# Kernel optimization log

Hardware: AMD Instinct MI355X
Metric: run time of the kernel (lower is better)

## Reference

```python
import jax, jax.numpy as jnp
import numpy as np
import math

L = 16
DECAY = math.exp(-1.0 / 10.0)   # exp(-dt/tau)
THRESHOLD = 1.0
ALPHA = 0.01
EPS = 1e-6


def spike_fn(x):
    # MultiBitSurrogate forward: floor then clamp to [0, L]
    return jnp.clip(jnp.floor(x), 0.0, float(L))


def setup_inputs() -> dict:
    key = jax.random.key(0)
    k1, k2 = jax.random.split(key)
    B, S, D, H = 8, 4096, 512, 512
    x = jax.random.normal(k1, (B, S, D), dtype=jnp.float32)
    W = jax.random.normal(k2, (H, D), dtype=jnp.float32) * (1.0 / math.sqrt(D))
    b = jnp.zeros((H,), dtype=jnp.float32)
    return {"x": x, "W": W, "b": b}


def reference(x, W, b):
    B, S, D = x.shape
    H = W.shape[0]
    # dense input current for all timesteps: (B, S, H)
    h = jnp.einsum('bsd,hd->bsh', x, W) + b

    v0 = jnp.zeros((B, H), dtype=x.dtype)
    theta0 = jnp.full((B, H), THRESHOLD, dtype=x.dtype)

    def step(carry, i_t):
        v, theta = carry
        v = v * DECAY + i_t
        clamp_limit = L * theta * 2.0
        v = jnp.clip(v, -clamp_limit, clamp_limit)
        normalized_v = v / (theta + EPS)
        spike = spike_fn(normalized_v)
        v = v - spike * theta
        theta = theta + ALPHA * spike - ALPHA * (theta - THRESHOLD)
        return (v, theta), spike

    h_t = jnp.swapaxes(h, 0, 1)  # (S, B, H) for scan over time
    (v, theta), spikes = jax.lax.scan(step, (v0, theta0), h_t)
    spikes = jnp.swapaxes(spikes, 0, 1)  # (B, S, H)
    return spikes, v, theta
```

## Files before the change

kernel.cpp:

```cpp
#include <hip/hip_runtime.h>

#define B_DIM 8
#define S_LEN 4096
#define D_DIM 512
#define H_DIM 512

#define DECAY_F 0.90483743f
#define ALPHA_F 0.01f
#define EPS_F   1e-6f

#define KT 16
#define NCHUNK (S_LEN / 32)
#define NSCAN_BLOCKS 64


__device__ __forceinline__ void stage_chunk(const float* __restrict__ gio, float* dstbase,
                                            int c, int lane) {
    const float* src = gio + (size_t)(c * 32 + (lane >> 4)) * H_DIM + ((lane & 15) << 2);
#pragma unroll
    for (int i = 0; i < 8; ++i) {
        __builtin_amdgcn_global_load_lds(
            (const __attribute__((address_space(1))) void*)(src + (size_t)i * 4 * H_DIM),
            (__attribute__((address_space(3))) void*)(dstbase + i * 256),
            16, 0, 0);
    }
}

__device__ __forceinline__ void gemm_tile(const float* __restrict__ x,
                                          const float* __restrict__ W,
                                          const float* __restrict__ bias,
                                          float* __restrict__ out,
                                          float (*As)[132], float (*Bs)[132],
                                          int bm, int bn) {
    const int tid = threadIdx.x;
    const int waveId = tid >> 6;
    const int waveR = waveId & 1;
    const int waveC = waveId >> 1;
    const int lane = tid & 63;
    const int tr = lane >> 3;
    const int tc = lane & 7;
    const int rbase = waveR * 64 + tr * 8;
    const int c0 = waveC * 64 + tc * 4;
    const int c1 = c0 + 32;

    const int lrow = tid >> 2;
    const int lk4  = (tid & 3) * 4;

    const float* xa = &x[(size_t)(bm + lrow) * D_DIM + lk4];
    const float* xb = &x[(size_t)(bm + lrow + 64) * D_DIM + lk4];
    const float* wa = &W[(size_t)(bn + lrow) * D_DIM + lk4];
    const float* wb = &W[(size_t)(bn + lrow + 64) * D_DIM + lk4];

    float acc[8][8];
#pragma unroll
    for (int i = 0; i < 8; ++i)
#pragma unroll
        for (int j = 0; j < 8; ++j) acc[i][j] = 0.f;

    float4 a0 = *reinterpret_cast<const float4*>(xa);
    float4 a1 = *reinterpret_cast<const float4*>(xb);
    float4 b0 = *reinterpret_cast<const float4*>(wa);
    float4 b1 = *reinterpret_cast<const float4*>(wb);

    for (int kk = 0; kk < D_DIM; kk += KT) {
        __syncthreads();
        As[lk4 + 0][lrow]      = a0.x;
        As[lk4 + 1][lrow]      = a0.y;
        As[lk4 + 2][lrow]      = a0.z;
        As[lk4 + 3][lrow]      = a0.w;
        As[lk4 + 0][lrow + 64] = a1.x;
        As[lk4 + 1][lrow + 64] = a1.y;
        As[lk4 + 2][lrow + 64] = a1.z;
        As[lk4 + 3][lrow + 64] = a1.w;
        Bs[lk4 + 0][lrow]      = b0.x;
        Bs[lk4 + 1][lrow]      = b0.y;
        Bs[lk4 + 2][lrow]      = b0.z;
        Bs[lk4 + 3][lrow]      = b0.w;
        Bs[lk4 + 0][lrow + 64] = b1.x;
        Bs[lk4 + 1][lrow + 64] = b1.y;
        Bs[lk4 + 2][lrow + 64] = b1.z;
        Bs[lk4 + 3][lrow + 64] = b1.w;
        __syncthreads();

        if (kk + KT < D_DIM) {
            a0 = *reinterpret_cast<const float4*>(xa + kk + KT);
            a1 = *reinterpret_cast<const float4*>(xb + kk + KT);
            b0 = *reinterpret_cast<const float4*>(wa + kk + KT);
            b1 = *reinterpret_cast<const float4*>(wb + kk + KT);
        }

#pragma unroll
        for (int k = 0; k < KT; ++k) {
            const float4 av0 = *reinterpret_cast<const float4*>(&As[k][rbase]);
            const float4 av1 = *reinterpret_cast<const float4*>(&As[k][rbase + 4]);
            const float4 bv0 = *reinterpret_cast<const float4*>(&Bs[k][c0]);
            const float4 bv1 = *reinterpret_cast<const float4*>(&Bs[k][c1]);
            const float am[8]  = {av0.x, av0.y, av0.z, av0.w, av1.x, av1.y, av1.z, av1.w};
            const float bn_[8] = {bv0.x, bv0.y, bv0.z, bv0.w, bv1.x, bv1.y, bv1.z, bv1.w};
#pragma unroll
            for (int i = 0; i < 8; ++i)
#pragma unroll
                for (int j = 0; j < 8; ++j) acc[i][j] += am[i] * bn_[j];
        }
    }

    const float4 bias0 = *reinterpret_cast<const float4*>(&bias[bn + c0]);
    const float4 bias1 = *reinterpret_cast<const float4*>(&bias[bn + c1]);
    const float bb[8] = {bias0.x, bias0.y, bias0.z, bias0.w, bias1.x, bias1.y, bias1.z, bias1.w};

#pragma unroll
    for (int i = 0; i < 8; ++i) {
        const size_t row = (size_t)(bm + rbase + i);
        float4 o0, o1;
        o0.x = acc[i][0] + bb[0]; o0.y = acc[i][1] + bb[1];
        o0.z = acc[i][2] + bb[2]; o0.w = acc[i][3] + bb[3];
        o1.x = acc[i][4] + bb[4]; o1.y = acc[i][5] + bb[5];
        o1.z = acc[i][6] + bb[6]; o1.w = acc[i][7] + bb[7];
        *reinterpret_cast<float4*>(&out[row * H_DIM + bn + c0]) = o0;
        *reinterpret_cast<float4*>(&out[row * H_DIM + bn + c1]) = o1;
    }
}

__device__ __forceinline__ void scan_wave(float* __restrict__ gio, float* sbuf,
                                          const int* flagrow, int lane,
                                          float* __restrict__ vout,
                                          float* __restrict__ thout, int chain) {
    float v = 0.f;
    float theta = 1.f;
    float tden = theta + EPS_F;
    float rs = __builtin_amdgcn_rcpf(tden);
    float es = fmaf(-tden, rs, 1.0f);
    float r1 = fmaf(es, rs, rs);
    float es2 = fmaf(-tden, r1, 1.0f);
    float r0 = fmaf(es2, r1, r1);
    float cl = 32.f * theta;
    const float kSixteen = 16.0f;

    if (flagrow) {
        while (__hip_atomic_load(&flagrow[0], __ATOMIC_ACQUIRE, __HIP_MEMORY_SCOPE_AGENT) < 4)
            __builtin_amdgcn_s_sleep(1);
    }
    stage_chunk(gio, sbuf, 0, lane);
    asm volatile("s_waitcnt vmcnt(0)" ::: "memory");

    for (int c = 0; c < NCHUNK; ++c) {
        if (c + 1 < NCHUNK) {
            if (((c + 1) & 3) == 0 && flagrow) {
                const int stn = (c + 1) >> 2;
                while (__hip_atomic_load(&flagrow[stn], __ATOMIC_ACQUIRE,
                                         __HIP_MEMORY_SCOPE_AGENT) < 4)
                    __builtin_amdgcn_s_sleep(1);
                asm volatile("s_waitcnt vmcnt(0)" ::: "memory");
                stage_chunk(gio, sbuf + ((c + 1) & 1) * 2048, c + 1, lane);
            } else {
                stage_chunk(gio, sbuf + ((c + 1) & 1) * 2048, c + 1, lane);
                asm volatile("s_waitcnt vmcnt(40)" ::: "memory");
            }
        } else {
            asm volatile("s_waitcnt vmcnt(32)" ::: "memory");
        }
        __builtin_amdgcn_sched_barrier(0);

        const float* sb = sbuf + (c & 1) * 2048 + lane;
        float rr[32];
#pragma unroll
        for (int i = 0; i < 32; ++i) rr[i] = sb[i * 64];
        __builtin_amdgcn_sched_barrier(0);

        float* gout = gio + (size_t)c * 32 * H_DIM + lane;

#pragma unroll
        for (int u = 0; u < 32; ++u) {
            float vv = v * DECAY_F + rr[u];
            asm("v_med3_f32 %0, %0, -%1, %1" : "+v"(vv) : "v"(cl));
            v = vv;

            const float q0 = v * r0;
            const float e1 = fmaf(-tden, q0, v);
            const float nv = fmaf(e1, r0, q0);

            float spike = floorf(nv);
            asm("v_med3_f32 %0, %0, 0, %1" : "+v"(spike) : "v"(kSixteen));

            v = v - spike * theta;
            theta = theta + ALPHA_F * spike - ALPHA_F * (theta - 1.0f);

            tden = theta + EPS_F;
            const float rrcp = __builtin_amdgcn_rcpf(tden);
            const float ee = fmaf(-tden, rrcp, 1.0f);
            const float ra = fmaf(ee, rrcp, rrcp);
            const float ee2 = fmaf(-tden, ra, 1.0f);
            r0 = fmaf(ee2, ra, ra);
            cl = 32.f * theta;

            gout[(size_t)u * H_DIM] = spike;
        }
        __builtin_amdgcn_sched_barrier(0);
    }

    vout[chain]  = v;
    thout[chain] = theta;
}

__global__ __launch_bounds__(256) void fused_kernel(const float* __restrict__ x,
                                                    const float* __restrict__ W,
                                                    const float* __restrict__ bias,
                                                    float* __restrict__ out,
                                                    float* __restrict__ vout,
                                                    float* __restrict__ thout,
                                                    int* __restrict__ flags) {
    __shared__ __align__(16) char smem_raw[16896];
    const int bid = blockIdx.x;

    if (bid >= NSCAN_BLOCKS) {
        float (*As)[132] = reinterpret_cast<float (*)[132]>(smem_raw);
        float (*Bs)[132] = reinterpret_cast<float (*)[132]>(smem_raw + sizeof(float) * KT * 132);

        const int g  = bid - NSCAN_BLOCKS;
        const int st = g >> 5;
        const int bb = (g >> 2) & 7;
        const int nt = g & 3;
        const int bm = bb * S_LEN + st * 128;
        const int bn = nt * 128;

        gemm_tile(x, W, bias, out, As, Bs, bm, bn);

        __syncthreads();
        if (threadIdx.x == 0) {
            __hip_atomic_fetch_add(&flags[bb * 32 + st], 1,
                                   __ATOMIC_RELEASE, __HIP_MEMORY_SCOPE_AGENT);
        }
        return;
    }

    if (threadIdx.x >= 64) return;
    __builtin_amdgcn_s_setprio(1);

    const int lane = threadIdx.x;
    const int gi   = bid;
    const int b    = gi >> 3;
    const int h0   = (gi & 7) << 6;

    float* sbuf = reinterpret_cast<float*>(smem_raw);
    const int* flagrow = flags + b * 32;
    float* gio = out + (size_t)b * S_LEN * H_DIM + h0;
    const int chain = b * H_DIM + h0 + lane;

    scan_wave(gio, sbuf, flagrow, lane, vout, thout, chain);
}


__global__ __launch_bounds__(256) void gemm_kernel(const float* __restrict__ x,
                                                   const float* __restrict__ W,
                                                   const float* __restrict__ bias,
                                                   float* __restrict__ out) {
    __shared__ float As[KT][132];
    __shared__ float Bs[KT][132];
    const int bm = blockIdx.y * 128;
    const int bn = blockIdx.x * 128;
    gemm_tile(x, W, bias, out, As, Bs, bm, bn);
}

__global__ __launch_bounds__(64, 1) void scan_kernel(float* __restrict__ io,
                                                     float* __restrict__ vout,
                                                     float* __restrict__ thout) {
    __shared__ float sbuf[2][32][64];
    const int lane = threadIdx.x;
    const int bi = blockIdx.x;
    const int b = bi >> 3;
    const int h0 = (bi & 7) << 6;
    float* gio = io + (size_t)b * S_LEN * H_DIM + h0;
    const int chain = b * H_DIM + h0 + lane;
    scan_wave(gio, &sbuf[0][0][0], nullptr, lane, vout, thout, chain);
}

extern "C" void kernel_launch(void* const* d_in, const int* in_sizes, int n_in,
                              void* d_out, int out_size, void* d_ws, size_t ws_size,
                              hipStream_t stream) {
    const float* x    = (const float*)d_in[0];
    const float* W    = (const float*)d_in[1];
    const float* bias = (const float*)d_in[2];

    float* out   = (float*)d_out;
    float* vout  = out + (size_t)B_DIM * S_LEN * H_DIM;
    float* thout = vout + B_DIM * H_DIM;

    if (ws_size >= 1024) {
        int* flags = (int*)d_ws;
        hipMemsetAsync(flags, 0, 256 * sizeof(int), stream);
        fused_kernel<<<NSCAN_BLOCKS + 1024, 256, 0, stream>>>(x, W, bias, out,
                                                              vout, thout, flags);
    } else {
        dim3 grid(H_DIM / 128, (B_DIM * S_LEN) / 128);
        gemm_kernel<<<grid, 256, 0, stream>>>(x, W, bias, out);
        scan_kernel<<<64, 64, 0, stream>>>(out, vout, thout);
    }
}
```

Before: 334.1 us.

## Interleave two scan chains per wave and halve scan block count

Each scan wave now carries two independent recurrence chains (128 hidden columns) instead of one, interleaving their steps to hide the serial dependency latency through instruction-level parallelism. The number of scan blocks drops from 64 to 32, and chunks shrink to 16 timesteps so the shared staging buffer keeps the same size. The cost is twice the serial work per wave, on half as many waves, with higher register pressure, so total scan latency depends on whether the dual-chain ILP hides the per-step latency.

```diff
diff --git a/kernel.cpp b/kernel.cpp
--- a/kernel.cpp
+++ b/kernel.cpp
@@ -10,21 +10,8 @@
 #define EPS_F   1e-6f
 
 #define KT 16
-#define NCHUNK (S_LEN / 32)
-#define NSCAN_BLOCKS 64
-
-
-__device__ __forceinline__ void stage_chunk(const float* __restrict__ gio, float* dstbase,
-                                            int c, int lane) {
-    const float* src = gio + (size_t)(c * 32 + (lane >> 4)) * H_DIM + ((lane & 15) << 2);
-#pragma unroll
-    for (int i = 0; i < 8; ++i) {
-        __builtin_amdgcn_global_load_lds(
-            (const __attribute__((address_space(1))) void*)(src + (size_t)i * 4 * H_DIM),
-            (__attribute__((address_space(3))) void*)(dstbase + i * 256),
-            16, 0, 0);
-    }
-}
+#define NCHUNK 256
+#define NSCAN_BLOCKS 32
 
 __device__ __forceinline__ void gemm_tile(const float* __restrict__ x,
                                           const float* __restrict__ W,
@@ -121,39 +108,56 @@
     }
 }
 
-__device__ __forceinline__ void scan_wave(float* __restrict__ gio, float* sbuf,
-                                          const int* flagrow, int lane,
-                                          float* __restrict__ vout,
-                                          float* __restrict__ thout, int chain) {
-    float v = 0.f;
-    float theta = 1.f;
-    float tden = theta + EPS_F;
-    float rs = __builtin_amdgcn_rcpf(tden);
-    float es = fmaf(-tden, rs, 1.0f);
-    float r1 = fmaf(es, rs, rs);
-    float es2 = fmaf(-tden, r1, 1.0f);
-    float r0 = fmaf(es2, r1, r1);
-    float cl = 32.f * theta;
+__device__ __forceinline__ void scan_block(float* __restrict__ gio,
+                                           float* sbuf, const int* flagrow, int lane,
+                                           float* __restrict__ vout,
+                                           float* __restrict__ thout, int chainA) {
+#define SSTATE(sfx)                                                   \
+    float v##sfx = 0.f;                                               \
+    float theta##sfx = 1.f;                                           \
+    float tden##sfx = theta##sfx + EPS_F;                             \
+    float rs##sfx = __builtin_amdgcn_rcpf(tden##sfx);                 \
+    float es##sfx = fmaf(-tden##sfx, rs##sfx, 1.0f);                  \
+    float r1##sfx = fmaf(es##sfx, rs##sfx, rs##sfx);                  \
+    float es2##sfx = fmaf(-tden##sfx, r1##sfx, 1.0f);                 \
+    float r0##sfx = fmaf(es2##sfx, r1##sfx, r1##sfx);                 \
+    float cl##sfx = 32.f * theta##sfx;
+    SSTATE(A)
+    SSTATE(B)
+#undef SSTATE
     const float kSixteen = 16.0f;
+
+#define STAGE16(DST, C)                                                              \
+    do {                                                                             \
+        const float* src_ = gio + (size_t)((C) * 16 + (lane >> 5)) * H_DIM           \
+                              + ((lane & 31) << 2);                                  \
+        _Pragma("unroll")                                                            \
+        for (int i_ = 0; i_ < 8; ++i_) {                                             \
+            __builtin_amdgcn_global_load_lds(                                        \
+                (const __attribute__((address_space(1))) void*)(src_ + (size_t)(2 * i_) * H_DIM), \
+                (__attribute__((address_space(3))) void*)((DST) + i_ * 256),         \
+                16, 0, 0);                                                           \
+        }                                                                            \
+    } while (0)
 
     if (flagrow) {
         while (__hip_atomic_load(&flagrow[0], __ATOMIC_ACQUIRE, __HIP_MEMORY_SCOPE_AGENT) < 4)
             __builtin_amdgcn_s_sleep(1);
     }
-    stage_chunk(gio, sbuf, 0, lane);
+    STAGE16(sbuf, 0);
     asm volatile("s_waitcnt vmcnt(0)" ::: "memory");
 
     for (int c = 0; c < NCHUNK; ++c) {
         if (c + 1 < NCHUNK) {
-            if (((c + 1) & 3) == 0 && flagrow) {
-                const int stn = (c + 1) >> 2;
+            if (((c + 1) & 7) == 0 && flagrow) {
+                const int stn = (c + 1) >> 3;
                 while (__hip_atomic_load(&flagrow[stn], __ATOMIC_ACQUIRE,
                                          __HIP_MEMORY_SCOPE_AGENT) < 4)
                     __builtin_amdgcn_s_sleep(1);
                 asm volatile("s_waitcnt vmcnt(0)" ::: "memory");
-                stage_chunk(gio, sbuf + ((c + 1) & 1) * 2048, c + 1, lane);
+                STAGE16(sbuf + ((c + 1) & 1) * 2048, c + 1);
             } else {
-                stage_chunk(gio, sbuf + ((c + 1) & 1) * 2048, c + 1, lane);
+                STAGE16(sbuf + ((c + 1) & 1) * 2048, c + 1);
                 asm volatile("s_waitcnt vmcnt(40)" ::: "memory");
             }
         } else {
@@ -162,44 +166,49 @@
         __builtin_amdgcn_sched_barrier(0);
 
         const float* sb = sbuf + (c & 1) * 2048 + lane;
-        float rr[32];
-#pragma unroll
-        for (int i = 0; i < 32; ++i) rr[i] = sb[i * 64];
+        float rrA[16], rrB[16];
+#pragma unroll
+        for (int i = 0; i < 16; ++i) { rrA[i] = sb[i * 128]; rrB[i] = sb[i * 128 + 64]; }
         __builtin_amdgcn_sched_barrier(0);
 
-        float* gout = gio + (size_t)c * 32 * H_DIM + lane;
-
-#pragma unroll
-        for (int u = 0; u < 32; ++u) {
-            float vv = v * DECAY_F + rr[u];
-            asm("v_med3_f32 %0, %0, -%1, %1" : "+v"(vv) : "v"(cl));
-            v = vv;
-
-            const float q0 = v * r0;
-            const float e1 = fmaf(-tden, q0, v);
-            const float nv = fmaf(e1, r0, q0);
-
-            float spike = floorf(nv);
-            asm("v_med3_f32 %0, %0, 0, %1" : "+v"(spike) : "v"(kSixteen));
-
-            v = v - spike * theta;
-            theta = theta + ALPHA_F * spike - ALPHA_F * (theta - 1.0f);
-
-            tden = theta + EPS_F;
-            const float rrcp = __builtin_amdgcn_rcpf(tden);
-            const float ee = fmaf(-tden, rrcp, 1.0f);
-            const float ra = fmaf(ee, rrcp, rrcp);
-            const float ee2 = fmaf(-tden, ra, 1.0f);
-            r0 = fmaf(ee2, ra, ra);
-            cl = 32.f * theta;
-
-            gout[(size_t)u * H_DIM] = spike;
-        }
+        float* goutA = gio + (size_t)c * 16 * H_DIM + lane;
+
+#define STEP(sfx, IT, OUT_EXPR)                                       \
+        do {                                                          \
+            float vv = v##sfx * DECAY_F + (IT);                       \
+            asm("v_med3_f32 %0, %0, -%1, %1" : "+v"(vv) : "v"(cl##sfx)); \
+            v##sfx = vv;                                              \
+            const float q0 = v##sfx * r0##sfx;                        \
+            const float e1 = fmaf(-tden##sfx, q0, v##sfx);            \
+            const float nv = fmaf(e1, r0##sfx, q0);                   \
+            float spike = floorf(nv);                                 \
+            asm("v_med3_f32 %0, %0, 0, %1" : "+v"(spike) : "v"(kSixteen)); \
+            v##sfx = v##sfx - spike * theta##sfx;                     \
+            theta##sfx = theta##sfx + ALPHA_F * spike - ALPHA_F * (theta##sfx - 1.0f); \
+            tden##sfx = theta##sfx + EPS_F;                           \
+            const float rrcp = __builtin_amdgcn_rcpf(tden##sfx);      \
+            const float ee = fmaf(-tden##sfx, rrcp, 1.0f);            \
+            const float ra = fmaf(ee, rrcp, rrcp);                    \
+            const float ee2 = fmaf(-tden##sfx, ra, 1.0f);             \
+            r0##sfx = fmaf(ee2, ra, ra);                              \
+            cl##sfx = 32.f * theta##sfx;                              \
+            (OUT_EXPR) = spike;                                       \
+        } while (0)
+
+#pragma unroll
+        for (int u = 0; u < 16; ++u) {
+            STEP(A, rrA[u], goutA[(size_t)u * H_DIM]);
+            STEP(B, rrB[u], goutA[(size_t)u * H_DIM + 64]);
+        }
+#undef STEP
         __builtin_amdgcn_sched_barrier(0);
     }
 
-    vout[chain]  = v;
-    thout[chain] = theta;
+    vout[chainA]        = vA;
+    thout[chainA]       = thetaA;
+    vout[chainA + 64]   = vB;
+    thout[chainA + 64]  = thetaB;
+#undef STAGE16
 }
 
 __global__ __launch_bounds__(256) void fused_kernel(const float* __restrict__ x,
@@ -237,16 +246,14 @@
     __builtin_amdgcn_s_setprio(1);
 
     const int lane = threadIdx.x;
-    const int gi   = bid;
-    const int b    = gi >> 3;
-    const int h0   = (gi & 7) << 6;
+    const int b  = bid >> 2;
+    const int hb = (bid & 3) << 7;
 
     float* sbuf = reinterpret_cast<float*>(smem_raw);
-    const int* flagrow = flags + b * 32;
-    float* gio = out + (size_t)b * S_LEN * H_DIM + h0;
-    const int chain = b * H_DIM + h0 + lane;
-
-    scan_wave(gio, sbuf, flagrow, lane, vout, thout, chain);
+    float* gio = out + (size_t)b * S_LEN * H_DIM + hb;
+    const int chainA = b * H_DIM + hb + lane;
+
+    scan_block(gio, sbuf, flags + b * 32, lane, vout, thout, chainA);
 }
 
 
@@ -261,17 +268,17 @@
     gemm_tile(x, W, bias, out, As, Bs, bm, bn);
 }
 
-__global__ __launch_bounds__(64, 1) void scan_kernel(float* __restrict__ io,
-                                                     float* __restrict__ vout,
-                                                     float* __restrict__ thout) {
-    __shared__ float sbuf[2][32][64];
+__global__ __launch_bounds__(64, 1) void scan_serial_kernel(float* __restrict__ io,
+                                                            float* __restrict__ vout,
+                                                            float* __restrict__ thout) {
+    __shared__ __align__(16) float sbuf[4096];
+    const int bid = blockIdx.x;
     const int lane = threadIdx.x;
-    const int bi = blockIdx.x;
-    const int b = bi >> 3;
-    const int h0 = (bi & 7) << 6;
-    float* gio = io + (size_t)b * S_LEN * H_DIM + h0;
-    const int chain = b * H_DIM + h0 + lane;
-    scan_wave(gio, &sbuf[0][0][0], nullptr, lane, vout, thout, chain);
+    const int b  = bid >> 2;
+    const int hb = (bid & 3) << 7;
+    float* gio = io + (size_t)b * S_LEN * H_DIM + hb;
+    const int chainA = b * H_DIM + hb + lane;
+    scan_block(gio, sbuf, nullptr, lane, vout, thout, chainA);
 }
 
 extern "C" void kernel_launch(void* const* d_in, const int* in_sizes, int n_in,
@@ -287,12 +294,12 @@
 
     if (ws_size >= 1024) {
         int* flags = (int*)d_ws;
-        hipMemsetAsync(flags, 0, 256 * sizeof(int), stream);
+        hipMemsetAsync(flags, 0, 1024, stream);
         fused_kernel<<<NSCAN_BLOCKS + 1024, 256, 0, stream>>>(x, W, bias, out,
                                                               vout, thout, flags);
     } else {
         dim3 grid(H_DIM / 128, (B_DIM * S_LEN) / 128);
         gemm_kernel<<<grid, 256, 0, stream>>>(x, W, bias, out);
-        scan_kernel<<<64, 64, 0, stream>>>(out, vout, thout);
-    }
-}
+        scan_serial_kernel<<<NSCAN_BLOCKS, 64, 0, stream>>>(out, vout, thout);
+    }
+}
```

New measurement: 471.1 us. 41.0% more time.
